# Kernel tuning notes

Measured on AMD Instinct MI355X. Metric: run time of the kernel, lower is better.

Reference implementation:

```python
import jax, jax.numpy as jnp
import numpy as np

IN_C, HID, OUT_C, N = 128, 128, 1, 8192


def setup_inputs() -> dict:
    key = jax.random.key(0)
    ks = jax.random.split(key, 16)
    s_in = 1.0 / np.sqrt(IN_C)
    s_h = 1.0 / np.sqrt(HID)
    inp = {
        "x": jax.random.normal(ks[0], (N, IN_C), dtype=jnp.float32),
        "Wq": jax.random.uniform(ks[1], (IN_C, HID), minval=-s_in, maxval=s_in),
        "bq": jnp.zeros((HID,), jnp.float32),
        "Wk": jax.random.uniform(ks[2], (IN_C, HID), minval=-s_in, maxval=s_in),
        "bk": jnp.zeros((HID,), jnp.float32),
        "Wv": jax.random.uniform(ks[3], (IN_C, HID), minval=-s_in, maxval=s_in),
        "bv": jnp.zeros((HID,), jnp.float32),
        "Wskip": jax.random.uniform(ks[4], (IN_C, HID), minval=-s_in, maxval=s_in),
        "bskip": jnp.zeros((HID,), jnp.float32),
        "W1": jax.random.uniform(ks[5], (HID, HID), minval=-s_h, maxval=s_h),
        "b1": jnp.zeros((HID,), jnp.float32),
        "W2": jax.random.uniform(ks[6], (HID, OUT_C), minval=-s_h, maxval=s_h),
        "b2": jnp.zeros((OUT_C,), jnp.float32),
        "k": 7,
    }
    return inp


def _transformer_conv(x, Wq, bq, Wk, bk, Wv, bv, Wskip, bskip):
    # PyG TransformerConv, heads=1, concat=False, root_weight=True, over a
    # complete graph (no self-loops) -> dense attention with masked diagonal.
    q = x @ Wq + bq  # [N, H]
    kk = x @ Wk + bk
    v = x @ Wv + bv
    d = q.shape[-1]
    scores = (q @ kk.T) / jnp.sqrt(jnp.asarray(d, q.dtype))  # [N, N]
    n = x.shape[0]
    eye = jnp.eye(n, dtype=bool)
    scores = jnp.where(eye, -jnp.inf, scores)
    attn = jax.nn.softmax(scores, axis=-1)
    out = attn @ v
    return out + x @ Wskip + bskip


def _knn_indices(h, k):
    # k nearest neighbors (excluding self) in squared-euclidean distance.
    sq = jnp.sum(h * h, axis=1)
    d2 = sq[:, None] + sq[None, :] - 2.0 * (h @ h.T)  # [N, N]
    n = h.shape[0]
    d2 = jnp.where(jnp.eye(n, dtype=bool), jnp.inf, d2)
    _, idx = jax.lax.top_k(-d2, k)  # [N, k] neighbor (source) indices
    return idx


def _gcn_conv(h, idx, W, b, k):
    # Each node has exactly k incoming edges + self-loop => gcn_norm weight
    # is uniformly 1/(k+1) on every edge.
    m = h @ W  # [N, d]
    agg = (m[idx].sum(axis=1) + m) / jnp.asarray(k + 1, h.dtype)
    return agg + b


def reference(x, Wq, bq, Wk, bk, Wv, bv, Wskip, bskip, W1, b1, W2, b2, k):
    h = _transformer_conv(x, Wq, bq, Wk, bk, Wv, bv, Wskip, bskip)  # [N, HID]
    idx = _knn_indices(h, k)  # KNNGraph(k) on embeddings
    h1 = jax.nn.relu(_gcn_conv(h, idx, W1, b1, k))
    out = _gcn_conv(h1, idx, W2, b2, k)  # [N, OUT_C]
    return out
```

## Files before the change

kernel.cpp:

```cpp
#include <hip/hip_runtime.h>
#include <cmath>


typedef unsigned short ushort_t;

constexpr int   NN    = 8192;
constexpr int   DD    = 128;
constexpr int   KNB   = 7;
constexpr int   NL    = 10;
constexpr int   NCAND = 12;
constexpr float SCALE = 0.088388347648318447f;

using bf16x8 = __attribute__((ext_vector_type(8))) short;
using f32x4  = __attribute__((ext_vector_type(4))) float;

#define MFMA16(a, b, c) __builtin_amdgcn_mfma_f32_16x16x32_bf16((a), (b), (c), 0, 0, 0)

__device__ __forceinline__ ushort_t f2b(float f) {
    union { float f; unsigned int u; } v; v.f = f;
    return (ushort_t)((v.u + 0x8000u) >> 16);
}
__device__ __forceinline__ float b2f(ushort_t h) {
    union { unsigned int u; float f; } v; v.u = ((unsigned int)h) << 16;
    return v.f;
}

__device__ __forceinline__ void gload16(const void* g, void* l) {
    __builtin_amdgcn_global_load_lds(
        (const __attribute__((address_space(1))) unsigned int*)g,
        (__attribute__((address_space(3))) unsigned int*)l, 16, 0, 0);
}

__device__ __forceinline__ unsigned umin_(unsigned a, unsigned b) { return a < b ? a : b; }
__device__ __forceinline__ unsigned umax_(unsigned a, unsigned b) { return a > b ? a : b; }

template<int K>
__device__ __forceinline__ void ins_asc(unsigned* a, unsigned x)
{
    #pragma unroll
    for (int p = K - 1; p >= 1; --p)
        a[p] = umin_(umax_(x, a[p - 1]), a[p]);
    a[0] = umin_(a[0], x);
}

__global__ __launch_bounds__(128)
void proj_kernel(const float* __restrict__ x,
                 const float* __restrict__ Wq, const float* __restrict__ bq,
                 const float* __restrict__ Wk, const float* __restrict__ bk,
                 const float* __restrict__ Wv, const float* __restrict__ bv,
                 const float* __restrict__ Ws, const float* __restrict__ bs,
                 ushort_t* __restrict__ Qhi, ushort_t* __restrict__ Qlo,
                 ushort_t* __restrict__ Khi, ushort_t* __restrict__ Klo,
                 float* __restrict__ Vf, float* __restrict__ HS)
{
    __shared__ float xs[4][DD];
    const int i0 = blockIdx.x * 4, t = threadIdx.x;
    #pragma unroll
    for (int r = 0; r < 4; ++r) xs[r][t] = x[(i0 + r) * DD + t];
    __syncthreads();
    float aq[4] = {0,0,0,0}, ak[4] = {0,0,0,0}, av[4] = {0,0,0,0}, ah[4] = {0,0,0,0};
    #pragma unroll 4
    for (int c = 0; c < DD; ++c) {
        const float wq = Wq[c * DD + t], wk = Wk[c * DD + t];
        const float wv = Wv[c * DD + t], ws = Ws[c * DD + t];
        #pragma unroll
        for (int r = 0; r < 4; ++r) {
            const float xv = xs[r][c];
            aq[r] = fmaf(xv, wq, aq[r]); ak[r] = fmaf(xv, wk, ak[r]);
            av[r] = fmaf(xv, wv, av[r]); ah[r] = fmaf(xv, ws, ah[r]);
        }
    }
    #pragma unroll
    for (int r = 0; r < 4; ++r) {
        const int o = (i0 + r) * DD + t;
        const float q = aq[r] + bq[t];
        const float k = ak[r] + bk[t];
        const ushort_t qh = f2b(q); Qhi[o] = qh; Qlo[o] = f2b(q - b2f(qh));
        const ushort_t kh = f2b(k); Khi[o] = kh; Klo[o] = f2b(k - b2f(kh));
        Vf[o] = av[r] + bv[t];
        HS[o] = ah[r] + bs[t];
    }
}

__global__ __launch_bounds__(256)
void vt_kernel(const float* __restrict__ Vf,
               ushort_t* __restrict__ VThi, ushort_t* __restrict__ VTlo)
{
    __shared__ float tile[64 * 132];
    const int k0 = blockIdx.x * 64, t = threadIdx.x;
    #pragma unroll
    for (int p = 0; p < 8; ++p) {
        const int slot = t + p * 256;
        const int r = slot >> 5, c4 = slot & 31;
        *reinterpret_cast<float4*>(&tile[r * 132 + c4 * 4]) =
            *reinterpret_cast<const float4*>(Vf + (k0 + r) * DD + c4 * 4);
    }
    __syncthreads();
    #pragma unroll
    for (int p = 0; p < 4; ++p) {
        const int slot = t + p * 256;
        const int f = slot >> 3, kc = slot & 7;
        ushort_t hh[8], ll[8];
        #pragma unroll
        for (int i = 0; i < 8; ++i) {
            const float v = tile[(kc * 8 + i) * 132 + f];
            hh[i] = f2b(v); ll[i] = f2b(v - b2f(hh[i]));
        }
        *reinterpret_cast<uint4*>(VThi + f * NN + k0 + kc * 8) =
            *reinterpret_cast<const uint4*>(hh);
        *reinterpret_cast<uint4*>(VTlo + f * NN + k0 + kc * 8) =
            *reinterpret_cast<const uint4*>(ll);
    }
}

constexpr int ANS  = 8;
constexpr int AKS  = NN / ANS;
constexpr int BK   = 32;
constexpr int PSTR = 40;
constexpr int KSTR = 136;

__global__ __launch_bounds__(256, 2)
void attn_kernel(const ushort_t* __restrict__ Qhi, const ushort_t* __restrict__ Qlo,
                 const ushort_t* __restrict__ Khg, const ushort_t* __restrict__ Klg,
                 const ushort_t* __restrict__ Vhg, const ushort_t* __restrict__ Vlg,
                 float* __restrict__ Opart, float* __restrict__ lpart)
{
    __shared__ __align__(16) ushort_t Khs[2][BK * DD];
    __shared__ __align__(16) ushort_t Kls[2][BK * DD];
    __shared__ __align__(16) ushort_t Vhs[2][DD * BK];
    __shared__ __align__(16) ushort_t Vls[2][DD * BK];
    __shared__ __align__(16) ushort_t Phs[4][16 * PSTR];
    __shared__ __align__(16) ushort_t Pls[4][16 * PSTR];

    const int t  = threadIdx.x;
    const int w  = t >> 6, l = t & 63;
    const int lc = l & 15, lq = l >> 4;
    const int b  = blockIdx.x;
    const int s  = b >> 6;
    const int qb = b & 63;
    const int i0 = qb * 128;
    const int k0 = s * AKS;
    ushort_t* Pwh = Phs[w];
    ushort_t* Pwl = Pls[w];

    const int lrK = w * 4 + (l >> 4);
    const int kchunk = ((l & 15) ^ (lrK & 7)) * 8;
    const ushort_t* gKh = Khg + (size_t)(k0 + lrK) * DD + kchunk;
    const ushort_t* gKl = Klg + (size_t)(k0 + lrK) * DD + kchunk;
    const int lrV = w * 16 + (l >> 2);
    const int vchunk = ((l & 3) ^ ((l >> 3) & 3)) * 8;
    const ushort_t* gVh = Vhg + (size_t)lrV * NN + k0 + vchunk;
    const ushort_t* gVl = Vlg + (size_t)lrV * NN + k0 + vchunk;

#define STAGE(buf, koff) do {                                              \
    gload16(gKh + (size_t)(koff) * DD,        &Khs[buf][(w * 4) * DD]);    \
    gload16(gKh + (size_t)((koff) + 16) * DD, &Khs[buf][(16 + w * 4) * DD]); \
    gload16(gKl + (size_t)(koff) * DD,        &Kls[buf][(w * 4) * DD]);    \
    gload16(gKl + (size_t)((koff) + 16) * DD, &Kls[buf][(16 + w * 4) * DD]); \
    gload16(gVh + (koff),                     &Vhs[buf][(w * 16) * BK]);   \
    gload16(gVh + (size_t)64 * NN + (koff),   &Vhs[buf][(64 + w * 16) * BK]); \
    gload16(gVl + (koff),                     &Vls[buf][(w * 16) * BK]);   \
    gload16(gVl + (size_t)64 * NN + (koff),   &Vls[buf][(64 + w * 16) * BK]); \
  } while (0)

    bf16x8 qh[2][4], ql[2][4];
    #pragma unroll
    for (int sub = 0; sub < 2; ++sub) {
        const int row = i0 + w * 32 + sub * 16 + lc;
        #pragma unroll
        for (int kb = 0; kb < 4; ++kb) {
            qh[sub][kb] = *reinterpret_cast<const bf16x8*>(Qhi + row * DD + kb * 32 + lq * 8);
            ql[sub][kb] = *reinterpret_cast<const bf16x8*>(Qlo + row * DD + kb * 32 + lq * 8);
        }
    }

    const f32x4 zz = {0.f, 0.f, 0.f, 0.f};
    f32x4 oacc[2][8];
    #pragma unroll
    for (int sub = 0; sub < 2; ++sub)
        #pragma unroll
        for (int ft = 0; ft < 8; ++ft) oacc[sub][ft] = zz;
    float lrow[2] = {0.f, 0.f};

    STAGE(0, 0);
    __syncthreads();

    constexpr int NT = AKS / BK;
    for (int it = 0; it < NT; ++it) {
        const int cur = it & 1;
        const int jt  = k0 + it * BK;

        if (it + 1 < NT) STAGE(cur ^ 1, (it + 1) * BK);

        const ushort_t* Kh = Khs[cur];
        const ushort_t* Kl = Kls[cur];
        const ushort_t* Vh = Vhs[cur];
        const ushort_t* Vl = Vls[cur];

        f32x4 sacc[2][2];
        #pragma unroll
        for (int sub = 0; sub < 2; ++sub)
            #pragma unroll
            for (int kt = 0; kt < 2; ++kt) sacc[sub][kt] = zz;
        __builtin_amdgcn_s_setprio(1);
        #pragma unroll
        for (int kt = 0; kt < 2; ++kt) {
            const int kro = (kt * 16 + lc) * DD;
            #pragma unroll
            for (int kb = 0; kb < 4; ++kb) {
                const int cp = ((kb * 4 + lq) ^ (lc & 7)) * 8;
                const bf16x8 kh = *reinterpret_cast<const bf16x8*>(&Kh[kro + cp]);
                const bf16x8 kl = *reinterpret_cast<const bf16x8*>(&Kl[kro + cp]);
                #pragma unroll
                for (int sub = 0; sub < 2; ++sub) {
                    sacc[sub][kt] = MFMA16(kh, qh[sub][kb], sacc[sub][kt]);
                    sacc[sub][kt] = MFMA16(kh, ql[sub][kb], sacc[sub][kt]);
                    sacc[sub][kt] = MFMA16(kl, qh[sub][kb], sacc[sub][kt]);
                }
            }
        }
        __builtin_amdgcn_s_setprio(0);
        if ((jt & ~127) == i0) {
            #pragma unroll
            for (int sub = 0; sub < 2; ++sub) {
                const int gq = i0 + w * 32 + sub * 16 + lc;
                #pragma unroll
                for (int kt = 0; kt < 2; ++kt)
                    #pragma unroll
                    for (int r = 0; r < 4; ++r) {
                        const int gk = jt + kt * 16 + lq * 4 + r;
                        if (gk == gq) sacc[sub][kt][r] = -INFINITY;
                    }
            }
        }
        bf16x8 pah[2], pal[2];
        #pragma unroll
        for (int sub = 0; sub < 2; ++sub) {
            #pragma unroll
            for (int kt = 0; kt < 2; ++kt) {
                unsigned wh[2], wl[2];
                #pragma unroll
                for (int rr = 0; rr < 2; ++rr) {
                    const float p0 = __expf(sacc[sub][kt][rr * 2 + 0] * SCALE);
                    const float p1 = __expf(sacc[sub][kt][rr * 2 + 1] * SCALE);
                    lrow[sub] += p0;
                    lrow[sub] += p1;
                    const ushort_t ph0 = f2b(p0), ph1 = f2b(p1);
                    wh[rr] = (unsigned)ph0 | ((unsigned)ph1 << 16);
                    wl[rr] = (unsigned)f2b(p0 - b2f(ph0)) |
                             ((unsigned)f2b(p1 - b2f(ph1)) << 16);
                }
                const int eo = lc * PSTR + kt * 16 + lq * 4;
                *reinterpret_cast<uint2*>(&Pwh[eo]) = make_uint2(wh[0], wh[1]);
                *reinterpret_cast<uint2*>(&Pwl[eo]) = make_uint2(wl[0], wl[1]);
            }
            pah[sub] = *reinterpret_cast<const bf16x8*>(&Pwh[lc * PSTR + lq * 8]);
            pal[sub] = *reinterpret_cast<const bf16x8*>(&Pwl[lc * PSTR + lq * 8]);
        }
        __builtin_amdgcn_s_setprio(1);
        #pragma unroll
        for (int ft = 0; ft < 8; ++ft) {
            const int vc = (lq ^ ((lc >> 1) & 3)) * 8;
            const bf16x8 vh = *reinterpret_cast<const bf16x8*>(
                &Vh[(ft * 16 + lc) * BK + vc]);
            const bf16x8 vl = *reinterpret_cast<const bf16x8*>(
                &Vl[(ft * 16 + lc) * BK + vc]);
            #pragma unroll
            for (int sub = 0; sub < 2; ++sub) {
                oacc[sub][ft] = MFMA16(pah[sub], vh, oacc[sub][ft]);
                oacc[sub][ft] = MFMA16(pal[sub], vh, oacc[sub][ft]);
                oacc[sub][ft] = MFMA16(pah[sub], vl, oacc[sub][ft]);
            }
        }
        __builtin_amdgcn_s_setprio(0);

        __syncthreads();
    }
#undef STAGE

    #pragma unroll
    for (int sub = 0; sub < 2; ++sub) {
        float ps = lrow[sub];
        ps += __shfl_xor(ps, 16, 64);
        ps += __shfl_xor(ps, 32, 64);
        lrow[sub] = ps;
    }
    #pragma unroll
    for (int sub = 0; sub < 2; ++sub) {
        #pragma unroll
        for (int r = 0; r < 4; ++r) {
            const int row = i0 + w * 32 + sub * 16 + lq * 4 + r;
            float* po = Opart + ((size_t)s * NN + row) * DD;
            #pragma unroll
            for (int ft = 0; ft < 8; ++ft) po[ft * 16 + lc] = oacc[sub][ft][r];
        }
        if (l < 16)
            lpart[s * NN + i0 + w * 32 + sub * 16 + l] = lrow[sub];
    }
}

__global__ __launch_bounds__(256)
void attn_merge_kernel(const float* __restrict__ Opart, const float* __restrict__ lpart,
                       const float* __restrict__ HS, float* __restrict__ H,
                       ushort_t* __restrict__ Hhi, float* __restrict__ SQ)
{
    const int t = threadIdx.x;
    const int gid = blockIdx.x * 256 + t;
    const int i = gid >> 5;
    const int f = (gid & 31) * 4;
    float ls = 0.f;
    float4 o = {0.f, 0.f, 0.f, 0.f};
    #pragma unroll
    for (int s = 0; s < ANS; ++s) {
        ls += lpart[s * NN + i];
        const float4 ov = *reinterpret_cast<const float4*>(
            Opart + ((size_t)s * NN + i) * DD + f);
        o.x += ov.x; o.y += ov.y; o.z += ov.z; o.w += ov.w;
    }
    const float4 hs = *reinterpret_cast<const float4*>(HS + i * DD + f);
    const float inv = 1.f / ls;
    float4 h;
    h.x = o.x * inv + hs.x; h.y = o.y * inv + hs.y;
    h.z = o.z * inv + hs.z; h.w = o.w * inv + hs.w;
    *reinterpret_cast<float4*>(H + i * DD + f) = h;
    ushort_t hb[4] = {f2b(h.x), f2b(h.y), f2b(h.z), f2b(h.w)};
    *reinterpret_cast<uint2*>(Hhi + i * DD + f) = *reinterpret_cast<const uint2*>(hb);
    float sq = h.x * h.x + h.y * h.y + h.z * h.z + h.w * h.w;
    sq += __shfl_xor(sq, 1, 64);
    sq += __shfl_xor(sq, 2, 64);
    sq += __shfl_xor(sq, 4, 64);
    sq += __shfl_xor(sq, 8, 64);
    sq += __shfl_xor(sq, 16, 64);
    if ((t & 31) == 0) SQ[i] = sq;
}

constexpr int KNSL = 16;
constexpr int KSL  = NN / KNSL;

__global__ __launch_bounds__(256, 4)
void knn_kernel(const ushort_t* __restrict__ Hhi, const float* __restrict__ SQg,
                unsigned* __restrict__ candV)
{
    __shared__ __align__(16) ushort_t Khi[64 * KSTR];
    __shared__ __align__(16) float sqs[64];

    const int t  = threadIdx.x;
    const int w  = t >> 6, l = t & 63;
    const int lc = l & 15, lq = l >> 4;
    const int b  = blockIdx.x;
    const int s  = b >> 6;
    const int qb = b & 63;
    const int i0 = qb * 128;
    const int k0 = s * KSL;

    const int kr = t >> 4, kc2 = t & 15;

    const int gq0 = i0 + w * 32 + lc;
    const int gq1 = gq0 + 16;
    const float sqi0 = SQg[gq0];
    const float sqi1 = SQg[gq1];

    bf16x8 qf[2][4];
    #pragma unroll
    for (int sub = 0; sub < 2; ++sub) {
        const int row = i0 + w * 32 + sub * 16 + lc;
        #pragma unroll
        for (int kb = 0; kb < 4; ++kb)
            qf[sub][kb] = *reinterpret_cast<const bf16x8*>(Hhi + row * DD + kb * 32 + lq * 8);
    }

    unsigned lists[2][NL];
    #pragma unroll
    for (int sub = 0; sub < 2; ++sub)
        #pragma unroll
        for (int p = 0; p < NL; ++p) lists[sub][p] = 0xFFFFFFFFu;

    uint4 pk[4]; float psq;
    #pragma unroll
    for (int p = 0; p < 4; ++p)
        pk[p] = *reinterpret_cast<const uint4*>(Hhi + (k0 + kr + p * 16) * DD + kc2 * 8);
    psq = (t < 64) ? SQg[k0 + t] : 0.f;

    const f32x4 zz = {0.f, 0.f, 0.f, 0.f};
    for (int jt0 = 0; jt0 < KSL; jt0 += 64) {
        const int jt = k0 + jt0;
        __syncthreads();
        #pragma unroll
        for (int p = 0; p < 4; ++p)
            *reinterpret_cast<uint4*>(&Khi[(kr + p * 16) * KSTR + kc2 * 8]) = pk[p];
        if (t < 64) sqs[t] = psq;
        __syncthreads();
        if (jt0 + 64 < KSL) {
            const int jn = jt + 64;
            #pragma unroll
            for (int p = 0; p < 4; ++p)
                pk[p] = *reinterpret_cast<const uint4*>(Hhi + (jn + kr + p * 16) * DD + kc2 * 8);
            psq = (t < 64) ? SQg[jn + t] : 0.f;
        }

        f32x4 acc[2][4];
        #pragma unroll
        for (int sub = 0; sub < 2; ++sub)
            #pragma unroll
            for (int kt = 0; kt < 4; ++kt) acc[sub][kt] = zz;
        #pragma unroll
        for (int kt = 0; kt < 4; ++kt) {
            #pragma unroll
            for (int kb = 0; kb < 4; ++kb) {
                const bf16x8 kf = *reinterpret_cast<const bf16x8*>(
                    &Khi[(kt * 16 + lc) * KSTR + kb * 32 + lq * 8]);
                acc[0][kt] = MFMA16(kf, qf[0][kb], acc[0][kt]);
                acc[1][kt] = MFMA16(kf, qf[1][kb], acc[1][kt]);
            }
        }

        const bool ovl = ((jt & ~127) == i0);
        #pragma unroll
        for (int kt = 0; kt < 4; ++kt) {
            const float4 sq4 = *reinterpret_cast<const float4*>(&sqs[kt * 16 + lq * 4]);
            const float sqj[4] = {sq4.x, sq4.y, sq4.z, sq4.w};
            #pragma unroll
            for (int r = 0; r < 4; ++r) {
                const int gk = jt + kt * 16 + lq * 4 + r;
                float d0 = fmaf(-2.f, acc[0][kt][r], sqi0 + sqj[r]);
                float d1 = fmaf(-2.f, acc[1][kt][r], sqi1 + sqj[r]);
                if (ovl) {
                    if (gk == gq0) d0 = INFINITY;
                    if (gk == gq1) d1 = INFINITY;
                }
                const unsigned u0 = (__float_as_uint(d0) & 0xFFFFE000u) | (unsigned)gk;
                const unsigned u1 = (__float_as_uint(d1) & 0xFFFFE000u) | (unsigned)gk;
                ins_asc<NL>(lists[0], u0);
                ins_asc<NL>(lists[1], u1);
            }
        }
    }

    __syncthreads();
    unsigned* msw = reinterpret_cast<unsigned*>(Khi) + w * (16 * 4 * NL);
    #pragma unroll
    for (int sub = 0; sub < 2; ++sub) {
        #pragma unroll
        for (int p = 0; p < NL; ++p)
            msw[lc * (4 * NL) + lq * NL + p] = lists[sub][p];
        __syncthreads();
        if (lq == 0) {
            unsigned bk[NL];
            #pragma unroll
            for (int p = 0; p < NL; ++p) bk[p] = msw[lc * (4 * NL) + p];
            #pragma unroll
            for (int o = 1; o < 4; ++o)
                #pragma unroll
                for (int e = 0; e < NL; ++e)
                    ins_asc<NL>(bk, msw[lc * (4 * NL) + o * NL + e]);
            const int node = i0 + w * 32 + sub * 16 + lc;
            #pragma unroll
            for (int p = 0; p < NL; ++p)
                candV[((size_t)s * NL + p) * NN + node] = bk[p];
        }
        __syncthreads();
    }
}

__global__ __launch_bounds__(64)
void knn_merge_kernel(const unsigned* __restrict__ candV, int* __restrict__ CAND)
{
    const int q = blockIdx.x * 64 + threadIdx.x;
    unsigned bk[NCAND];
    #pragma unroll
    for (int p = 0; p < NCAND; ++p) bk[p] = 0xFFFFFFFFu;
    for (int s = 0; s < KNSL; ++s)
        #pragma unroll
        for (int e = 0; e < NL; ++e)
            ins_asc<NCAND>(bk, candV[((size_t)s * NL + e) * NN + q]);
    #pragma unroll
    for (int p = 0; p < NCAND; ++p)
        CAND[q * NCAND + p] = (int)(bk[p] & 8191u);
}

__global__ __launch_bounds__(256)
void rerank_kernel(const float* __restrict__ H, const float* __restrict__ SQ,
                   const int* __restrict__ CAND, int* __restrict__ IDX)
{
    const int t = threadIdx.x;
    const int w = t >> 6, l = t & 63;
    const int node = blockIdx.x * 4 + w;
    const float h0 = H[node * DD + l];
    const float h1 = H[node * DD + 64 + l];
    float dk[NCAND]; int di[NCAND];
    #pragma unroll
    for (int c = 0; c < NCAND; ++c) {
        const int j = CAND[node * NCAND + c];
        float p = h0 * H[j * DD + l] + h1 * H[j * DD + 64 + l];
        p += __shfl_xor(p, 1, 64);
        p += __shfl_xor(p, 2, 64);
        p += __shfl_xor(p, 4, 64);
        p += __shfl_xor(p, 8, 64);
        p += __shfl_xor(p, 16, 64);
        p += __shfl_xor(p, 32, 64);
        dk[c] = SQ[j] - 2.f * p;
        di[c] = j;
    }
    if (l == 0) {
        #pragma unroll
        for (int s = 0; s < KNB; ++s) {
            int best = s;
            #pragma unroll
            for (int c = s + 1; c < NCAND; ++c) {
                const bool lt = (dk[c] < dk[best]) ||
                                (dk[c] == dk[best] && di[c] < di[best]);
                if (lt) best = c;
            }
            const float tk = dk[s]; dk[s] = dk[best]; dk[best] = tk;
            const int   ti = di[s]; di[s] = di[best]; di[best] = ti;
            IDX[node * KNB + s] = di[s];
        }
    }
}

__global__ __launch_bounds__(128)
void mat1_kernel(const float* __restrict__ Hin, const float* __restrict__ W,
                 float* __restrict__ M)
{
    __shared__ float xs[4][DD];
    const int i0 = blockIdx.x * 4, t = threadIdx.x;
    #pragma unroll
    for (int r = 0; r < 4; ++r) xs[r][t] = Hin[(i0 + r) * DD + t];
    __syncthreads();
    float a[4] = {0,0,0,0};
    #pragma unroll 4
    for (int c = 0; c < DD; ++c) {
        const float wv = W[c * DD + t];
        #pragma unroll
        for (int r = 0; r < 4; ++r) a[r] = fmaf(xs[r][c], wv, a[r]);
    }
    #pragma unroll
    for (int r = 0; r < 4; ++r) M[(i0 + r) * DD + t] = a[r];
}

__global__ __launch_bounds__(128)
void g1m2_kernel(const float* __restrict__ M1, const int* __restrict__ IDX,
                 const float* __restrict__ b1, const float* __restrict__ W2,
                 float* __restrict__ M2)
{
    __shared__ float red[128];
    const int i = blockIdx.x, t = threadIdx.x;
    float s = M1[i * DD + t];
    #pragma unroll
    for (int p = 0; p < KNB; ++p) s += M1[IDX[i * KNB + p] * DD + t];
    const float h1 = fmaxf(s * 0.125f + b1[t], 0.f);
    red[t] = h1 * W2[t];
    __syncthreads();
    for (int s2 = 64; s2 > 0; s2 >>= 1) {
        if (t < s2) red[t] += red[t + s2];
        __syncthreads();
    }
    if (t == 0) M2[i] = red[0];
}

__global__ __launch_bounds__(256)
void out_kernel(const float* __restrict__ M2, const int* __restrict__ IDX,
                const float* __restrict__ b2, float* __restrict__ out)
{
    const int i = blockIdx.x * 256 + threadIdx.x;
    if (i < NN) {
        float s = M2[i];
        #pragma unroll
        for (int p = 0; p < KNB; ++p) s += M2[IDX[i * KNB + p]];
        out[i] = s * 0.125f + b2[0];
    }
}

extern "C" void kernel_launch(void* const* d_in, const int* in_sizes, int n_in,
                              void* d_out, int out_size, void* d_ws, size_t ws_size,
                              hipStream_t stream)
{
    const float* x   = (const float*)d_in[0];
    const float* Wq  = (const float*)d_in[1];
    const float* bq  = (const float*)d_in[2];
    const float* Wk  = (const float*)d_in[3];
    const float* bk  = (const float*)d_in[4];
    const float* Wv  = (const float*)d_in[5];
    const float* bv  = (const float*)d_in[6];
    const float* Wsk = (const float*)d_in[7];
    const float* bsk = (const float*)d_in[8];
    const float* W1  = (const float*)d_in[9];
    const float* b1  = (const float*)d_in[10];
    const float* W2  = (const float*)d_in[11];
    const float* b2  = (const float*)d_in[12];

    constexpr size_t MB = 1024 * 1024;
    char* W = (char*)d_ws;
    ushort_t* Qhi  = (ushort_t*)(W + 0 * MB);
    ushort_t* Qlo  = (ushort_t*)(W + 2 * MB);
    ushort_t* Khi  = (ushort_t*)(W + 4 * MB);
    ushort_t* Klo  = (ushort_t*)(W + 6 * MB);
    ushort_t* VThi = (ushort_t*)(W + 8 * MB);
    ushort_t* VTlo = (ushort_t*)(W + 10 * MB);
    float*    HS   = (float*)(W + 12 * MB);
    float*    H    = HS;
    ushort_t* Hhi  = Qhi;
    float* lpart = (float*)(W + 16 * MB);
    float* SQ    = (float*)(W + 16 * MB + 256 * 1024);
    float* M2    = SQ + NN;
    int*   IDX   = (int*)(M2 + NN);
    float*    Vf32  = (float*)(W + 17 * MB);
    float*    Opart = (float*)(W + 17 * MB);
    unsigned* candV = (unsigned*)(W + 17 * MB);
    int*      CAND  = (int*)(W + 23 * MB);
    float*    M1    = (float*)(W + 24 * MB);

    proj_kernel<<<NN / 4, 128, 0, stream>>>(x, Wq, bq, Wk, bk, Wv, bv, Wsk, bsk,
                                            Qhi, Qlo, Khi, Klo, Vf32, HS);
    vt_kernel<<<NN / 64, 256, 0, stream>>>(Vf32, VThi, VTlo);
    attn_kernel<<<ANS * 64, 256, 0, stream>>>(Qhi, Qlo, Khi, Klo, VThi, VTlo,
                                              Opart, lpart);
    attn_merge_kernel<<<(NN * 32) / 256, 256, 0, stream>>>(Opart, lpart, HS, H,
                                                           Hhi, SQ);
    knn_kernel<<<KNSL * 64, 256, 0, stream>>>(Hhi, SQ, candV);
    knn_merge_kernel<<<NN / 64, 64, 0, stream>>>(candV, CAND);
    rerank_kernel<<<NN / 4, 256, 0, stream>>>(H, SQ, CAND, IDX);
    mat1_kernel<<<NN / 4, 128, 0, stream>>>(H, W1, M1);
    g1m2_kernel<<<NN, 128, 0, stream>>>(M1, IDX, b1, W2, M2);
    out_kernel<<<NN / 256, 256, 0, stream>>>(M2, IDX, b2, (float*)d_out);
}
```

Baseline: 339.2 us.

## Software-pipeline attention PV matmul one tile behind QK scores

Splits tile staging into separate K and V loads. The P·V MFMA pass for the previous tile now runs right after the current tile's QK MFMAs, and the final tile's P·V is drained after the loop. The point is to let the exp/softmax VALU work and LDS P round-trip overlap with matrix-core work from a different iteration, instead of running them strictly in sequence. In exchange, P fragments stay live across iterations (more registers), V is staged one iteration later with a shorter prefetch lead, and the extra epilogue adds code size.

```diff
diff --git a/kernel.cpp b/kernel.cpp
--- a/kernel.cpp
+++ b/kernel.cpp
@@ -152,15 +152,17 @@
     const ushort_t* gVh = Vhg + (size_t)lrV * NN + k0 + vchunk;
     const ushort_t* gVl = Vlg + (size_t)lrV * NN + k0 + vchunk;
 
-#define STAGE(buf, koff) do {                                              \
-    gload16(gKh + (size_t)(koff) * DD,        &Khs[buf][(w * 4) * DD]);    \
+#define STAGE_K(buf, koff) do {                                              \
+    gload16(gKh + (size_t)(koff) * DD,        &Khs[buf][(w * 4) * DD]);      \
     gload16(gKh + (size_t)((koff) + 16) * DD, &Khs[buf][(16 + w * 4) * DD]); \
-    gload16(gKl + (size_t)(koff) * DD,        &Kls[buf][(w * 4) * DD]);    \
+    gload16(gKl + (size_t)(koff) * DD,        &Kls[buf][(w * 4) * DD]);      \
     gload16(gKl + (size_t)((koff) + 16) * DD, &Kls[buf][(16 + w * 4) * DD]); \
-    gload16(gVh + (koff),                     &Vhs[buf][(w * 16) * BK]);   \
-    gload16(gVh + (size_t)64 * NN + (koff),   &Vhs[buf][(64 + w * 16) * BK]); \
-    gload16(gVl + (koff),                     &Vls[buf][(w * 16) * BK]);   \
-    gload16(gVl + (size_t)64 * NN + (koff),   &Vls[buf][(64 + w * 16) * BK]); \
+  } while (0)
+#define STAGE_V(buf, koff) do {                                              \
+    gload16(gVh + (koff),                     &Vhs[buf][(w * 16) * BK]);     \
+    gload16(gVh + (size_t)64 * NN + (koff),   &Vhs[buf][(64 + w * 16) * BK]);\
+    gload16(gVl + (koff),                     &Vls[buf][(w * 16) * BK]);     \
+    gload16(gVl + (size_t)64 * NN + (koff),   &Vls[buf][(64 + w * 16) * BK]);\
   } while (0)
 
     bf16x8 qh[2][4], ql[2][4];
@@ -182,7 +184,10 @@
         for (int ft = 0; ft < 8; ++ft) oacc[sub][ft] = zz;
     float lrow[2] = {0.f, 0.f};
 
-    STAGE(0, 0);
+    bf16x8 pah[2] = {}, pal[2] = {};
+    const int vc = (lq ^ ((lc >> 1) & 3)) * 8;
+
+    STAGE_K(0, 0);
     __syncthreads();
 
     constexpr int NT = AKS / BK;
@@ -190,12 +195,11 @@
         const int cur = it & 1;
         const int jt  = k0 + it * BK;
 
-        if (it + 1 < NT) STAGE(cur ^ 1, (it + 1) * BK);
+        if (it + 1 < NT) STAGE_K(cur ^ 1, (it + 1) * BK);
+        STAGE_V(cur, it * BK);
 
         const ushort_t* Kh = Khs[cur];
         const ushort_t* Kl = Kls[cur];
-        const ushort_t* Vh = Vhs[cur];
-        const ushort_t* Vl = Vls[cur];
 
         f32x4 sacc[2][2];
         #pragma unroll
@@ -220,6 +224,27 @@
             }
         }
         __builtin_amdgcn_s_setprio(0);
+
+        if (it > 0) {
+            const ushort_t* Vh = Vhs[cur ^ 1];
+            const ushort_t* Vl = Vls[cur ^ 1];
+            __builtin_amdgcn_s_setprio(1);
+            #pragma unroll
+            for (int ft = 0; ft < 8; ++ft) {
+                const bf16x8 vh = *reinterpret_cast<const bf16x8*>(
+                    &Vh[(ft * 16 + lc) * BK + vc]);
+                const bf16x8 vl = *reinterpret_cast<const bf16x8*>(
+                    &Vl[(ft * 16 + lc) * BK + vc]);
+                #pragma unroll
+                for (int sub = 0; sub < 2; ++sub) {
+                    oacc[sub][ft] = MFMA16(pah[sub], vh, oacc[sub][ft]);
+                    oacc[sub][ft] = MFMA16(pal[sub], vh, oacc[sub][ft]);
+                    oacc[sub][ft] = MFMA16(pah[sub], vl, oacc[sub][ft]);
+                }
+            }
+            __builtin_amdgcn_s_setprio(0);
+        }
+
         if ((jt & ~127) == i0) {
             #pragma unroll
             for (int sub = 0; sub < 2; ++sub) {
@@ -233,7 +258,6 @@
                     }
             }
         }
-        bf16x8 pah[2], pal[2];
         #pragma unroll
         for (int sub = 0; sub < 2; ++sub) {
             #pragma unroll
@@ -257,10 +281,14 @@
             pah[sub] = *reinterpret_cast<const bf16x8*>(&Pwh[lc * PSTR + lq * 8]);
             pal[sub] = *reinterpret_cast<const bf16x8*>(&Pwl[lc * PSTR + lq * 8]);
         }
-        __builtin_amdgcn_s_setprio(1);
+
+        __syncthreads();
+    }
+    {
+        const ushort_t* Vh = Vhs[(NT - 1) & 1];
+        const ushort_t* Vl = Vls[(NT - 1) & 1];
         #pragma unroll
         for (int ft = 0; ft < 8; ++ft) {
-            const int vc = (lq ^ ((lc >> 1) & 3)) * 8;
             const bf16x8 vh = *reinterpret_cast<const bf16x8*>(
                 &Vh[(ft * 16 + lc) * BK + vc]);
             const bf16x8 vl = *reinterpret_cast<const bf16x8*>(
@@ -272,11 +300,9 @@
                 oacc[sub][ft] = MFMA16(pah[sub], vl, oacc[sub][ft]);
             }
         }
-        __builtin_amdgcn_s_setprio(0);
-
-        __syncthreads();
-    }
-#undef STAGE
+    }
+#undef STAGE_K
+#undef STAGE_V
 
     #pragma unroll
     for (int sub = 0; sub < 2; ++sub) {
```

New measurement: 335.3 us. Within noise of the previous version (-1.1%).
